# Optimization experiments

Measured on AMD Instinct MI355X. Metric: run time of the kernel, lower is better.

## Reference

```python
import jax, jax.numpy as jnp
import numpy as np

N = 20000   # nodes
G = 8       # graphs
NP = N // G # nodes per graph
DEG = 32    # avg degree = avg_num_neighbors
E = N * DEG # edges
C = 64      # channels (features_dim, hidden 0e/1o multiplicity)
S = 8       # num_species
NB = 8      # num bessel basis
L = 3       # nlayers
CUT = 6.0
AVG = 32.0


def setup_inputs() -> dict:
    rng = np.random.default_rng(0)
    # edges strictly within each graph, sender != receiver (guarantees nonzero lengths a.s.)
    il = rng.integers(0, NP, E)
    off = rng.integers(1, NP, E)
    ge = rng.integers(0, G, E)
    base = ge * NP
    edge_index = jnp.asarray(np.stack([base + il, base + (il + off) % NP]).astype(np.int64))
    batch = jnp.asarray(np.repeat(np.arange(G), NP).astype(np.int64))
    species = jnp.asarray(rng.integers(0, S, N).astype(np.int64))
    pos = jnp.asarray((rng.random((N, 3)) * 10.0).astype(np.float32))
    cell = jnp.asarray((10.0 * np.eye(3)[None] + 0.1 * rng.standard_normal((G, 3, 3))).astype(np.float32))
    Sij = jnp.asarray(rng.integers(-1, 2, (E, 3)).astype(np.float32))
    ks = jax.random.split(jax.random.key(0), 16)
    def w(k, shape, fan):
        return jax.random.normal(k, shape, jnp.float32) / np.sqrt(fan).astype(np.float32)
    return dict(
        pos=pos, cell=cell, Sij=Sij,
        W_embed=w(ks[0], (S, C), S), W_x=w(ks[1], (C, C), C),
        W_up_s=w(ks[2], (L, C, C), C), W_up_v=w(ks[3], (L, C, C), C),
        Wr1=w(ks[4], (L, NB, 64), NB), br1=jnp.zeros((L, 64), jnp.float32),
        Wr2=w(ks[5], (L, 64, 64), 64), br2=jnp.zeros((L, 64), jnp.float32),
        Wr3=w(ks[6], (L, 64, 4 * C), 64),
        W_msg_s=w(ks[7], (L, C, C), C), W_msg_v=w(ks[8], (L, C, C), C),
        W_sc_s=w(ks[9], (L, S, C, C), C), W_sc_v=w(ks[10], (L, S, C, C), C),
        W_p_s=w(ks[11], (L, C, C), C), W_p_v=w(ks[12], (L, C, C), C),
        W_read=w(ks[13], (L, 3, C), C),
        edge_index=edge_index, batch=batch, species=species,
    )


def _forward(pos, cell, Sij, W_embed, W_x, W_up_s, W_up_v, Wr1, br1, Wr2, br2, Wr3,
             W_msg_s, W_msg_v, W_sc_s, W_sc_v, W_p_s, W_p_v, W_read,
             edge_index, batch, species):
    snd, rcv = edge_index[0], edge_index[1]
    # PBC shift vectors: per-edge einsum with that edge's graph cell (== per-graph split einsum)
    shift = jnp.einsum('ei,eij->ej', Sij, cell[batch[snd]])
    Rij = (pos[rcv] - pos[snd] + shift) / CUT
    lengths = jnp.linalg.norm(Rij, axis=1)
    mask = (lengths > 0).astype(pos.dtype)  # zero-length edge masking (in place of boolean filter)
    safe = jnp.where(lengths > 0, lengths, 1.0)
    # spherical harmonics up to l=1, component normalization on unit vectors
    y1 = jnp.sqrt(3.0) * Rij / safe[:, None]
    # bessel radial basis (r_max=1 since lengths pre-scaled by cutoff) + polynomial cutoff p=2
    nfreq = jnp.arange(1, NB + 1, dtype=pos.dtype)
    bess = jnp.sqrt(2.0) * jnp.sin(jnp.pi * nfreq * safe[:, None]) / safe[:, None]
    xl = safe
    env = jnp.where(xl < 1.0, 1.0 - 6.0 * xl**2 + 8.0 * xl**3 - 3.0 * xl**4, 0.0)
    edge_feats = bess * (env * mask)[:, None]  # [E, NB]
    attrs = jax.nn.one_hot(species, S, dtype=pos.dtype)  # [N, S]
    s = attrs @ W_embed                      # scalar features [N, C]
    v = jnp.zeros((s.shape[0], C, 3), s.dtype)  # vector features [N, C, 3]
    xf = s @ W_x                             # linear_x residual features
    inv_sqrt3 = 1.0 / jnp.sqrt(3.0)
    outs = []
    for l in range(L):
        s_up = s @ W_up_s[l]
        v_up = jnp.einsum('ncm,co->nom', v, W_up_v[l])
        # radial MLP -> per-edge tensor-product path weights [E, 4, C]
        h = jax.nn.silu(edge_feats @ Wr1[l] + br1[l])
        h = jax.nn.silu(h @ Wr2[l] + br2[l])
        wts = (h @ Wr3[l]).reshape(-1, 4, C) * mask[:, None, None]
        ss, vv = s_up[snd], v_up[snd]
        # equivariant message paths: 0x0->0, 1x1->0 (dot), 0x1->1, 1x0->1
        m_s = wts[:, 0] * ss + wts[:, 1] * (jnp.einsum('ecm,em->ec', vv, y1) * inv_sqrt3)
        m_v = wts[:, 2][:, :, None] * ss[:, :, None] * y1[:, None, :] + wts[:, 3][:, :, None] * vv
        agg_s = jax.ops.segment_sum(m_s, rcv, num_segments=s.shape[0]) / AVG
        agg_v = jax.ops.segment_sum(m_v, rcv, num_segments=s.shape[0]) / AVG
        msg_s = agg_s @ W_msg_s[l]
        msg_v = jnp.einsum('ncm,co->nom', agg_v, W_msg_v[l])
        # species-conditioned skip connection (sc)
        sc_s = jnp.einsum('nk,nc,kco->no', attrs, s, W_sc_s[l])
        sc_v = jnp.einsum('nk,ncm,kco->nom', attrs, v, W_sc_v[l])
        # product block: depthwise product with x_node_feats, linear mix, + sc
        s = (xf * msg_s) @ W_p_s[l] + sc_s
        v = jnp.einsum('ncm,co->nom', xf[:, :, None] * msg_v, W_p_v[l]) + sc_v
        # readout: hidden -> 3x1o = 9 values per node
        outs.append(jnp.einsum('ncm,oc->nom', v, W_read[l]).reshape(-1, 9))
    node_e = jax.nn.silu(jnp.stack(outs, -1)).sum(-1)          # [N, 9]
    graph_e = jax.ops.segment_sum(node_e, batch, num_segments=G)
    return graph_e.reshape(G, 3, 3)


def reference(pos, cell, Sij, W_embed, W_x, W_up_s, W_up_v, Wr1, br1, Wr2, br2, Wr3,
              W_msg_s, W_msg_v, W_sc_s, W_sc_v, W_p_s, W_p_v, W_read,
              edge_index, batch, species):
    return _forward(pos, cell, Sij, W_embed, W_x, W_up_s, W_up_v, Wr1, br1, Wr2, br2, Wr3,
                    W_msg_s, W_msg_v, W_sc_s, W_sc_v, W_p_s, W_p_v, W_read,
                    edge_index, batch, species)
```

## Files before the change

### kernel.cpp

```cpp
#include <hip/hip_runtime.h>
#include <math.h>

#define NN 20000
#define GG 8
#define NPG 2500
#define EE 640000
#define EPAD 944000
#define NLAYERS 3
#define CUTR 6.0f
#define AVGN 32.0f
#define NBASIS 8
#define WPL 22528
#define RTS 88

#define LDS_HANDOFF() do { \
    asm volatile("s_waitcnt lgkmcnt(0)" ::: "memory"); \
    __builtin_amdgcn_sched_barrier(0); \
  } while (0)

typedef short bf16x8 __attribute__((ext_vector_type(8)));
typedef _Float16 f16x8 __attribute__((ext_vector_type(8)));
typedef float f32x4 __attribute__((ext_vector_type(4)));

__device__ __forceinline__ float silu_f(float x){ return x / (1.0f + __expf(-x)); }
__device__ __forceinline__ unsigned short f2h(float f){
  union { _Float16 h; unsigned short u; } x; x.h = (_Float16)f;
  return x.u;
}

__global__ void k_count(const int* __restrict__ ei, int* __restrict__ deg)
{
  int e = blockIdx.x * 256 + threadIdx.x;
  if (e >= EE) return;
  atomicAdd(&deg[ei[EE + e]], 1);
}

__global__ void k_scan(const int* __restrict__ deg, int* __restrict__ rowptrP,
                       int* __restrict__ cursor)
{
  __shared__ int buf[1024];
  __shared__ int carry;
  int tid = threadIdx.x;
  if (tid == 0) carry = 0;
  __syncthreads();
  for (int base = 0; base < NN; base += 1024) {
    int i = base + tid;
    int x = (i < NN) ? ((deg[i] + 15) & ~15) : 0;
    buf[tid] = x; __syncthreads();
    for (int off = 1; off < 1024; off <<= 1) {
      int t = (tid >= off) ? buf[tid - off] : 0;
      __syncthreads();
      buf[tid] += t;
      __syncthreads();
    }
    int incl = buf[tid];
    int c = carry;
    __syncthreads();
    if (i < NN) { rowptrP[i] = c + incl - x; cursor[i] = c + incl - x; }
    if (tid == 1023) carry = c + incl;
    __syncthreads();
  }
  if (tid == 0) rowptrP[NN] = carry;
}

__global__ void k_scatter(const int* __restrict__ ei, int* __restrict__ cursor,
                          unsigned* __restrict__ csrE)
{
  int e = blockIdx.x * 256 + threadIdx.x;
  if (e >= EE) return;
  int slot = atomicAdd(&cursor[ei[EE + e]], 1);
  csrE[slot] = (unsigned)e;
}

__global__ __launch_bounds__(512) void k_sortrows(const int* __restrict__ rowptrP,
                                                  unsigned* __restrict__ csrE)
{
  __shared__ unsigned buf[8*512];
  int w = threadIdx.x >> 6, lane = threadIdx.x & 63;
  unsigned* b = buf + w*512;
  int r = blockIdx.x*8 + w;
  int start = rowptrP[r], end = rowptrP[r+1];
  int P = end - start;
  if (P < 2 || P > 512) return;
  for (int i = lane; i < P; i += 64) b[i] = csrE[start + i];
  LDS_HANDOFF();
  for (int pass = 0; pass < P; ++pass) {
    int par = pass & 1;
    for (int i = lane; 2*i + par + 1 < P; i += 64) {
      int idx = 2*i + par;
      unsigned a = b[idx], c = b[idx+1];
      if (a > c) { b[idx] = c; b[idx+1] = a; }
    }
    LDS_HANDOFF();
  }
  for (int i = lane; i < P; i += 64) csrE[start + i] = b[i];
}

__global__ void k_geom_slot(const float* __restrict__ pos, const float* __restrict__ cell,
                            const float* __restrict__ Sij, const int* __restrict__ ei,
                            const int* __restrict__ batch, const unsigned* __restrict__ csrE,
                            unsigned short* __restrict__ efeatH, float* __restrict__ y1mP,
                            int* __restrict__ sndP)
{
  int slot = blockIdx.x * 256 + threadIdx.x;
  if (slot >= EPAD) return;
  int e = (int)csrE[slot];
  if (e < 0) {
    ((uint4*)efeatH)[slot] = make_uint4(0,0,0,0);
    ((float4*)y1mP)[slot]  = make_float4(0,0,0,0);
    sndP[slot] = 0;
    return;
  }
  int snd = ei[e], rcv = ei[EE + e];
  int g = batch[snd];
  float s0 = Sij[e*3+0], s1 = Sij[e*3+1], s2_ = Sij[e*3+2];
  const float* cg = cell + g*9;
  float R[3];
  #pragma unroll
  for (int j = 0; j < 3; ++j) {
    float shift = s0*cg[0*3+j] + s1*cg[1*3+j] + s2_*cg[2*3+j];
    R[j] = (pos[rcv*3+j] - pos[snd*3+j] + shift) * (1.0f/CUTR);
  }
  float len = sqrtf(R[0]*R[0] + R[1]*R[1] + R[2]*R[2]);
  float mk   = (len > 0.0f) ? 1.0f : 0.0f;
  float safe = (len > 0.0f) ? len  : 1.0f;
  float inv  = 1.0f / safe;
  const float sqrt3 = 1.7320508075688772f;
  float x = safe;
  float env = (x < 1.0f) ? (1.0f - 6.0f*x*x + 8.0f*x*x*x - 3.0f*x*x*x*x) : 0.0f;
  float emk = env * mk;
  const float sqrt2 = 1.4142135623730951f;
  const float PI_F = 3.14159265358979323846f;
  union { unsigned short u[8]; uint4 q; } fb;
  #pragma unroll
  for (int n = 1; n <= NBASIS; ++n)
    fb.u[n-1] = f2h(sqrt2 * __sinf(PI_F * (float)n * safe) * inv * emk);
  ((uint4*)efeatH)[slot] = fb.q;
  ((float4*)y1mP)[slot]  = make_float4(sqrt3*R[0]*inv, sqrt3*R[1]*inv, sqrt3*R[2]*inv, mk);
  sndP[slot] = snd;
}

__global__ void k_wprep(const float* __restrict__ Wr1, const float* __restrict__ Wr2,
                        const float* __restrict__ Wr3, unsigned short* __restrict__ wfrag)
{
  int gid = blockIdx.x * 256 + threadIdx.x;
  if (gid >= 3 * WPL) return;
  int l = gid / WPL, r = gid % WPL;
  float val;
  if (r < 2048) {
    int f = r >> 9, wi = r & 511, L = wi >> 3, j = wi & 7;
    int k = (L >> 4) * 8 + j, n = L & 15, ct = f;
    val = (k < 8) ? Wr1[l*512 + k*64 + ct*16 + n] : 0.0f;
  } else if (r < 6144) {
    int r2 = r - 2048;
    int f = r2 >> 9, wi = r2 & 511, L = wi >> 3, j = wi & 7;
    int kt = f >> 2, ct = f & 3;
    int k = kt*32 + (L >> 4)*8 + j, n = L & 15;
    val = Wr2[l*4096 + k*64 + ct*16 + n];
  } else {
    int r3 = r - 6144;
    int f = r3 >> 9, wi = r3 & 511, L = wi >> 3, j = wi & 7;
    int kt = f >> 4, ct = f & 15;
    int k = kt*32 + (L >> 4)*8 + j, n = L & 15;
    val = Wr3[l*16384 + k*256 + ct*16 + n];
  }
  wfrag[gid] = f2h(val);
}

__global__ void k_embed0(const int* __restrict__ species, const float* __restrict__ W_embed,
                         const float* __restrict__ W_x, const float* __restrict__ Wus0,
                         float* __restrict__ T,
                         float* __restrict__ s, float* __restrict__ v,
                         float4* __restrict__ nodeP, float* __restrict__ acc_out)
{
  if (blockIdx.x == 0) {
    for (int t = threadIdx.x; t < 512; t += 256) {
      int sp = t >> 6, o = t & 63;
      float a = 0.0f;
      for (int k = 0; k < 64; ++k) a += W_embed[sp*64 + k] * W_x[k*64 + o];
      T[t] = a;
    }
  }
  int gid = blockIdx.x * 256 + threadIdx.x;
  if (gid >= NN * 64) return;
  int n = gid >> 6, c = gid & 63;
  int sp = species[n];
  s[gid] = W_embed[sp*64 + c];
  float up = 0.0f;
  for (int k = 0; k < 64; ++k) up += W_embed[sp*64 + k] * Wus0[k*64 + c];
  nodeP[gid] = make_float4(up, 0.0f, 0.0f, 0.0f);
  #pragma unroll
  for (int m = 0; m < 3; ++m) v[(n*3 + m)*64 + c] = 0.0f;
  if (c < 9) acc_out[n*9 + c] = 0.0f;
}

__global__ __launch_bounds__(512, 2) void k_gather(
    const int* __restrict__ rowptrP,
    const unsigned short* __restrict__ efeatH, const float4* __restrict__ y1mP,
    const int* __restrict__ sndP, const float4* __restrict__ nodeP,
    const unsigned short* __restrict__ wfrag,
    const float* __restrict__ br1, const float* __restrict__ br2,
    float4* __restrict__ aggP)
{
  __shared__ unsigned short smw[WPL];
  __shared__ float smf[128];
  __shared__ unsigned short rtAll[8*16*RTS];
  __shared__ float4 ymAll[8*16];
  __shared__ int sndAll[8*16];
  int tid = threadIdx.x;
  if (tid < 64) { smf[tid] = br1[tid]; smf[64+tid] = br2[tid]; }
  {
    const unsigned* src = (const unsigned*)wfrag;
    unsigned* dst = (unsigned*)smw;
    for (int i = tid; i < WPL/2; i += 512) dst[i] = src[i];
  }
  __syncthreads();
  const unsigned short* Wr1f = smw;
  const unsigned short* Wr2f = smw + 2048;
  const unsigned short* Wr3f = smw + 6144;

  int w = tid >> 6, lane = tid & 63;
  int n16 = lane & 15, quad = lane >> 4;
  unsigned short* rt = rtAll + w*16*RTS;
  float4* ym = ymAll + w*16;
  int* sndL = sndAll + w*16;
  int g = blockIdx.x & 7, rr = (blockIdx.x >> 3)*8 + w;
  if (rr < NPG) {
  int r = g*NPG + rr;
  int start = rowptrP[r], end = rowptrP[r+1];
  float as[4] = {0,0,0,0};
  float av[4][3] = {{0,0,0},{0,0,0},{0,0,0},{0,0,0}};
  const float inv_sqrt3 = 0.5773502691896258f;

  for (int e0 = start; e0 < end; e0 += 16) {
    if (quad == 1) ym[n16] = y1mP[e0 + n16];
    if (quad == 2) sndL[n16] = sndP[e0 + n16];
    LDS_HANDOFF();
    float4 np[4][4];
    #pragma unroll
    for (int ctm = 0; ctm < 4; ++ctm)
      #pragma unroll
      for (int j = 0; j < 4; ++j)
        np[ctm][j] = nodeP[(size_t)sndL[quad*4 + j]*64 + ctm*16 + n16];
    f16x8 aef = {0,0,0,0,0,0,0,0};
    if (quad == 0)
      aef = *(const f16x8*)(efeatH + (size_t)(e0 + n16)*8);
    f32x4 hacc[4];
    #pragma unroll
    for (int ct = 0; ct < 4; ++ct) {
      f16x8 bf = *(const f16x8*)(Wr1f + (ct*64 + lane)*8);
      hacc[ct] = __builtin_amdgcn_mfma_f32_16x16x32_f16(aef, bf, (f32x4){0,0,0,0}, 0, 0, 0);
    }
    #pragma unroll
    for (int ct = 0; ct < 4; ++ct) {
      int ch = ct*16 + n16;
      float b = smf[ch];
      #pragma unroll
      for (int reg = 0; reg < 4; ++reg)
        rt[(quad*4 + reg)*RTS + ch] = f2h(silu_f(hacc[ct][reg] + b));
    }
    LDS_HANDOFF();
    f16x8 a1[2];
    #pragma unroll
    for (int kt = 0; kt < 2; ++kt)
      a1[kt] = *(const f16x8*)(rt + n16*RTS + kt*32 + quad*8);
    LDS_HANDOFF();
    #pragma unroll
    for (int ct = 0; ct < 4; ++ct) {
      f16x8 b0 = *(const f16x8*)(Wr2f + ((0*4 + ct)*64 + lane)*8);
      f16x8 b1 = *(const f16x8*)(Wr2f + ((1*4 + ct)*64 + lane)*8);
      f32x4 acc = __builtin_amdgcn_mfma_f32_16x16x32_f16(a1[0], b0, (f32x4){0,0,0,0}, 0, 0, 0);
      hacc[ct]  = __builtin_amdgcn_mfma_f32_16x16x32_f16(a1[1], b1, acc, 0, 0, 0);
    }
    #pragma unroll
    for (int ct = 0; ct < 4; ++ct) {
      int ch = ct*16 + n16;
      float b = smf[64 + ch];
      #pragma unroll
      for (int reg = 0; reg < 4; ++reg) {
        float mkr = ym[quad*4 + reg].w;
        rt[(quad*4 + reg)*RTS + ch] = f2h(silu_f(hacc[ct][reg] + b) * mkr);
      }
    }
    LDS_HANDOFF();
    f16x8 a2[2];
    #pragma unroll
    for (int kt = 0; kt < 2; ++kt)
      a2[kt] = *(const f16x8*)(rt + n16*RTS + kt*32 + quad*8);
    #pragma unroll
    for (int ctm = 0; ctm < 4; ++ctm) {
      f32x4 wacc[4];
      #pragma unroll
      for (int p = 0; p < 4; ++p) {
        int ct = p*4 + ctm;
        f32x4 acc = __builtin_amdgcn_mfma_f32_16x16x32_f16(
            a2[0], *(const f16x8*)(Wr3f + ((0*16 + ct)*64 + lane)*8), (f32x4){0,0,0,0}, 0, 0, 0);
        wacc[p] = __builtin_amdgcn_mfma_f32_16x16x32_f16(
            a2[1], *(const f16x8*)(Wr3f + ((1*16 + ct)*64 + lane)*8), acc, 0, 0, 0);
      }
      #pragma unroll
      for (int j = 0; j < 4; ++j) {
        float4 y = ym[quad*4 + j];
        float4 npv = np[ctm][j];
        float dot = npv.y*y.x + npv.z*y.y + npv.w*y.z;
        float t2 = wacc[2][j]*npv.x;
        as[ctm]    += wacc[0][j]*npv.x + wacc[1][j]*dot*inv_sqrt3;
        av[ctm][0] += t2*y.x + wacc[3][j]*npv.y;
        av[ctm][1] += t2*y.y + wacc[3][j]*npv.z;
        av[ctm][2] += t2*y.z + wacc[3][j]*npv.w;
      }
      __builtin_amdgcn_sched_barrier(0);
    }
    LDS_HANDOFF();
  }
  const float invavg = 1.0f / AVGN;
  #pragma unroll
  for (int ctm = 0; ctm < 4; ++ctm) {
    float v0 = as[ctm], v1 = av[ctm][0], v2 = av[ctm][1], v3 = av[ctm][2];
    v0 += __shfl_xor(v0, 16); v0 += __shfl_xor(v0, 32);
    v1 += __shfl_xor(v1, 16); v1 += __shfl_xor(v1, 32);
    v2 += __shfl_xor(v2, 16); v2 += __shfl_xor(v2, 32);
    v3 += __shfl_xor(v3, 16); v3 += __shfl_xor(v3, 32);
    if (quad == 0)
      aggP[(size_t)r*64 + ctm*16 + n16] =
          make_float4(v0*invavg, v1*invavg, v2*invavg, v3*invavg);
  }
  }
}

__global__ __launch_bounds__(512) void k_post(
    const float4* __restrict__ aggP, const int* __restrict__ species,
    const float* __restrict__ T,
    float* __restrict__ s, float* __restrict__ v,
    const float* __restrict__ Wms, const float* __restrict__ Wmv,
    const float* __restrict__ Wscs, const float* __restrict__ Wscv,
    const float* __restrict__ Wps, const float* __restrict__ Wpv,
    const float* __restrict__ Wread,
    const float* __restrict__ Wus_n, const float* __restrict__ Wuv_n,
    float4* __restrict__ nodeP, float* __restrict__ acc_out, int has_next)
{
  __shared__ float lds[8*1024];
  int tid = threadIdx.x; int w = tid >> 6, c = tid & 63;
  float* asb = lds + w*1024;
  float* avb = asb + 64;
  float* sob = avb + 192;
  float* vob = sob + 64;
  float* tsb = vob + 192;
  float* tvb = tsb + 64;
  float* snb = tvb + 192;
  float* vnb = snb + 64;
  int n = blockIdx.x*8 + w;
  int sp = species[n];
  float4 ag = aggP[(size_t)n*64 + c];
  asb[c] = ag.x; avb[c] = ag.y; avb[64+c] = ag.z; avb[128+c] = ag.w;
  sob[c] = s[n*64 + c];
  #pragma unroll
  for (int m = 0; m < 3; ++m) vob[m*64 + c] = v[(n*3 + m)*64 + c];
  __syncthreads();
  float ms = 0, mv0 = 0, mv1 = 0, mv2 = 0;
  for (int k = 0; k < 64; ++k) {
    float wm = Wms[k*64 + c];
    ms  += asb[k]*wm;
    float wv = Wmv[k*64 + c];
    mv0 += avb[k]*wv; mv1 += avb[64+k]*wv; mv2 += avb[128+k]*wv;
  }
  float xf = T[sp*64 + c];
  tsb[c] = xf*ms; tvb[c] = xf*mv0; tvb[64+c] = xf*mv1; tvb[128+c] = xf*mv2;
  __syncthreads();
  const float* Wss = Wscs + sp*4096;
  const float* Wsv = Wscv + sp*4096;
  float sn_ = 0, vn0 = 0, vn1 = 0, vn2 = 0;
  for (int k = 0; k < 64; ++k) {
    float wp  = Wps[k*64 + c];  sn_ += tsb[k]*wp;
    float wsc = Wss[k*64 + c];  sn_ += sob[k]*wsc;
    float wpv = Wpv[k*64 + c];
    vn0 += tvb[k]*wpv; vn1 += tvb[64+k]*wpv; vn2 += tvb[128+k]*wpv;
    float wsv = Wsv[k*64 + c];
    vn0 += vob[k]*wsv; vn1 += vob[64+k]*wsv; vn2 += vob[128+k]*wsv;
  }
  s[n*64 + c] = sn_;
  v[(n*3+0)*64 + c] = vn0; v[(n*3+1)*64 + c] = vn1; v[(n*3+2)*64 + c] = vn2;
  snb[c] = sn_; vnb[c] = vn0; vnb[64+c] = vn1; vnb[128+c] = vn2;
  __syncthreads();
  if (c < 9) {
    int o3 = c / 3, m = c % 3;
    const float* wr = Wread + o3*64;
    float a = 0.0f;
    for (int k = 0; k < 64; ++k) a += vnb[m*64 + k]*wr[k];
    acc_out[n*9 + c] += silu_f(a);
  }
  if (has_next) {
    float su = 0, u0 = 0, u1 = 0, u2 = 0;
    for (int k = 0; k < 64; ++k) {
      float wu = Wus_n[k*64 + c]; su += snb[k]*wu;
      float wv = Wuv_n[k*64 + c];
      u0 += vnb[k]*wv; u1 += vnb[64+k]*wv; u2 += vnb[128+k]*wv;
    }
    nodeP[(size_t)n*64 + c] = make_float4(su, u0, u1, u2);
  }
}

__global__ void k_final(const float* __restrict__ acc_out, float* __restrict__ out)
{
  __shared__ float red[256];
  int g = blockIdx.x / 9, j = blockIdx.x % 9;
  int tid = threadIdx.x;
  float a = 0.0f;
  for (int n = g*NPG + tid; n < (g + 1)*NPG; n += 256) a += acc_out[n*9 + j];
  red[tid] = a; __syncthreads();
  for (int off = 128; off > 0; off >>= 1) {
    if (tid < off) red[tid] += red[tid + off];
    __syncthreads();
  }
  if (tid == 0) out[g*9 + j] = red[0];
}

extern "C" void kernel_launch(void* const* d_in, const int* in_sizes, int n_in,
                              void* d_out, int out_size, void* d_ws, size_t ws_size,
                              hipStream_t stream)
{
  const float* pos     = (const float*)d_in[0];
  const float* cell    = (const float*)d_in[1];
  const float* Sij     = (const float*)d_in[2];
  const float* W_embed = (const float*)d_in[3];
  const float* W_x     = (const float*)d_in[4];
  const float* W_up_s  = (const float*)d_in[5];
  const float* W_up_v  = (const float*)d_in[6];
  const float* Wr1     = (const float*)d_in[7];
  const float* br1     = (const float*)d_in[8];
  const float* Wr2     = (const float*)d_in[9];
  const float* br2     = (const float*)d_in[10];
  const float* Wr3     = (const float*)d_in[11];
  const float* W_msg_s = (const float*)d_in[12];
  const float* W_msg_v = (const float*)d_in[13];
  const float* W_sc_s  = (const float*)d_in[14];
  const float* W_sc_v  = (const float*)d_in[15];
  const float* W_p_s   = (const float*)d_in[16];
  const float* W_p_v   = (const float*)d_in[17];
  const float* W_read  = (const float*)d_in[18];
  const int*   ei      = (const int*)d_in[19];
  const int*   batch   = (const int*)d_in[20];
  const int*   species = (const int*)d_in[21];
  float* out = (float*)d_out;

  char* ws = (char*)d_ws;
  size_t off = 0;
  auto alloc = [&](size_t bytes) -> void* {
    void* p = ws + off;
    off += (bytes + 255) & ~(size_t)255;
    return p;
  };
  unsigned short* efeatH = (unsigned short*)alloc((size_t)EPAD*8*2);
  float* y1mP    = (float*)alloc((size_t)EPAD*4*4);
  int*   sndP    = (int*)alloc((size_t)EPAD*4);
  unsigned* csrE = (unsigned*)alloc((size_t)EPAD*4);
  float* sF      = (float*)alloc((size_t)NN*64*4);
  float* vF      = (float*)alloc((size_t)NN*192*4);
  float4* nodeP  = (float4*)alloc((size_t)NN*64*16);
  float4* aggP   = (float4*)alloc((size_t)NN*64*16);
  float* acc_out = (float*)alloc((size_t)NN*9*4);
  float* T       = (float*)alloc(512*4);
  unsigned short* wfrag = (unsigned short*)alloc((size_t)3*WPL*2);
  int* deg     = (int*)alloc((size_t)NN*4);
  int* rowptrP = (int*)alloc((size_t)(NN+1)*4);
  int* cursor  = (int*)alloc((size_t)NN*4);

  hipMemsetAsync(deg, 0, (size_t)NN*4, stream);
  hipMemsetAsync(csrE, 0xFF, (size_t)EPAD*4, stream);

  k_count<<<EE/256, 256, 0, stream>>>(ei, deg);
  k_scan <<<1, 1024, 0, stream>>>(deg, rowptrP, cursor);
  k_scatter <<<EE/256, 256, 0, stream>>>(ei, cursor, csrE);
  k_sortrows<<<NN/8, 512, 0, stream>>>(rowptrP, csrE);
  k_geom_slot<<<(EPAD+255)/256, 256, 0, stream>>>(pos, cell, Sij, ei, batch, csrE,
                                                  efeatH, y1mP, sndP);
  k_wprep <<<(3*WPL)/256, 256, 0, stream>>>(Wr1, Wr2, Wr3, wfrag);
  k_embed0<<<NN*64/256, 256, 0, stream>>>(species, W_embed, W_x, W_up_s, T,
                                          sF, vF, nodeP, acc_out);

  const int GATHER_BLOCKS = 8 * ((NPG + 7) / 8);
  for (int l = 0; l < NLAYERS; ++l) {
    k_gather<<<GATHER_BLOCKS, 512, 0, stream>>>(rowptrP, efeatH, (const float4*)y1mP, sndP,
                                                nodeP, wfrag + l*WPL, br1 + l*64, br2 + l*64,
                                                aggP);
    int has_next = (l < NLAYERS-1) ? 1 : 0;
    const float* Wus_n = W_up_s + (has_next ? (l+1)*4096 : l*4096);
    const float* Wuv_n = W_up_v + (has_next ? (l+1)*4096 : l*4096);
    k_post<<<2500, 512, 0, stream>>>(aggP, species, T, sF, vF,
                                     W_msg_s + l*4096, W_msg_v + l*4096,
                                     W_sc_s + l*32768, W_sc_v + l*32768,
                                     W_p_s + l*4096, W_p_v + l*4096,
                                     W_read + l*192, Wus_n, Wuv_n,
                                     nodeP, acc_out, has_next);
  }
  k_final<<<72, 256, 0, stream>>>(acc_out, out);
}
```

Measured before the change: 1.103 ms.

## Replace per-edge radial MLP with precomputed lookup table and linear interpolation

The radial MLP (Bessel basis, two hidden layers, output weights) depends only on edge length, so it is now tabulated per layer at 4097 points in a setup kernel. The gather kernel linearly interpolates these table entries instead of running three MFMA layers per edge tile. This removes the per-edge MFMA work, the LDS weight staging and the fp16 feature buffer. In exchange it adds random table reads, a 4 MB table per layer that should stay cache-resident, and a small interpolation error.

Result: faster. 916.5 us (median of 3 runs) (-16.9%).

```diff
diff --git a/kernel.cpp b/kernel.cpp
--- a/kernel.cpp
+++ b/kernel.cpp
@@ -10,23 +10,14 @@
 #define CUTR 6.0f
 #define AVGN 32.0f
 #define NBASIS 8
-#define WPL 22528
-#define RTS 88
+#define NT 4096
 
 #define LDS_HANDOFF() do { \
     asm volatile("s_waitcnt lgkmcnt(0)" ::: "memory"); \
     __builtin_amdgcn_sched_barrier(0); \
   } while (0)
 
-typedef short bf16x8 __attribute__((ext_vector_type(8)));
-typedef _Float16 f16x8 __attribute__((ext_vector_type(8)));
-typedef float f32x4 __attribute__((ext_vector_type(4)));
-
 __device__ __forceinline__ float silu_f(float x){ return x / (1.0f + __expf(-x)); }
-__device__ __forceinline__ unsigned short f2h(float f){
-  union { _Float16 h; unsigned short u; } x; x.h = (_Float16)f;
-  return x.u;
-}
 
 __global__ void k_count(const int* __restrict__ ei, int* __restrict__ deg)
 {
@@ -99,15 +90,13 @@
 __global__ void k_geom_slot(const float* __restrict__ pos, const float* __restrict__ cell,
                             const float* __restrict__ Sij, const int* __restrict__ ei,
                             const int* __restrict__ batch, const unsigned* __restrict__ csrE,
-                            unsigned short* __restrict__ efeatH, float* __restrict__ y1mP,
-                            int* __restrict__ sndP)
+                            float* __restrict__ y1mP, int* __restrict__ sndP)
 {
   int slot = blockIdx.x * 256 + threadIdx.x;
   if (slot >= EPAD) return;
   int e = (int)csrE[slot];
   if (e < 0) {
-    ((uint4*)efeatH)[slot] = make_uint4(0,0,0,0);
-    ((float4*)y1mP)[slot]  = make_float4(0,0,0,0);
+    ((float4*)y1mP)[slot] = make_float4(0.0f, 0.0f, 0.0f, -1.0f);
     sndP[slot] = 0;
     return;
   }
@@ -122,49 +111,50 @@
     R[j] = (pos[rcv*3+j] - pos[snd*3+j] + shift) * (1.0f/CUTR);
   }
   float len = sqrtf(R[0]*R[0] + R[1]*R[1] + R[2]*R[2]);
-  float mk   = (len > 0.0f) ? 1.0f : 0.0f;
-  float safe = (len > 0.0f) ? len  : 1.0f;
+  float safe = (len > 0.0f) ? len : 1.0f;
   float inv  = 1.0f / safe;
   const float sqrt3 = 1.7320508075688772f;
-  float x = safe;
-  float env = (x < 1.0f) ? (1.0f - 6.0f*x*x + 8.0f*x*x*x - 3.0f*x*x*x*x) : 0.0f;
-  float emk = env * mk;
+  float rq = (len > 0.0f) ? fminf(len, 1.0f) : -1.0f;
+  ((float4*)y1mP)[slot] = make_float4(sqrt3*R[0]*inv, sqrt3*R[1]*inv, sqrt3*R[2]*inv, rq);
+  sndP[slot] = snd;
+}
+
+__global__ __launch_bounds__(64) void k_tab(const float* __restrict__ Wr1, const float* __restrict__ br1,
+                                            const float* __restrict__ Wr2, const float* __restrict__ br2,
+                                            const float* __restrict__ Wr3, float4* __restrict__ Twts)
+{
+  __shared__ float h1s[64], h2s[64];
+  int l  = blockIdx.x / (NT+1);
+  int ip = blockIdx.x - l*(NT+1);
+  int c  = threadIdx.x;
+  float r  = (float)ip / (float)NT;
+  float re = fmaxf(r, 1e-7f);
+  float env = (r < 1.0f) ? (1.0f - 6.0f*r*r + 8.0f*r*r*r - 3.0f*r*r*r*r) : 0.0f;
   const float sqrt2 = 1.4142135623730951f;
   const float PI_F = 3.14159265358979323846f;
-  union { unsigned short u[8]; uint4 q; } fb;
+  float ef[NBASIS];
   #pragma unroll
   for (int n = 1; n <= NBASIS; ++n)
-    fb.u[n-1] = f2h(sqrt2 * __sinf(PI_F * (float)n * safe) * inv * emk);
-  ((uint4*)efeatH)[slot] = fb.q;
-  ((float4*)y1mP)[slot]  = make_float4(sqrt3*R[0]*inv, sqrt3*R[1]*inv, sqrt3*R[2]*inv, mk);
-  sndP[slot] = snd;
-}
-
-__global__ void k_wprep(const float* __restrict__ Wr1, const float* __restrict__ Wr2,
-                        const float* __restrict__ Wr3, unsigned short* __restrict__ wfrag)
-{
-  int gid = blockIdx.x * 256 + threadIdx.x;
-  if (gid >= 3 * WPL) return;
-  int l = gid / WPL, r = gid % WPL;
-  float val;
-  if (r < 2048) {
-    int f = r >> 9, wi = r & 511, L = wi >> 3, j = wi & 7;
-    int k = (L >> 4) * 8 + j, n = L & 15, ct = f;
-    val = (k < 8) ? Wr1[l*512 + k*64 + ct*16 + n] : 0.0f;
-  } else if (r < 6144) {
-    int r2 = r - 2048;
-    int f = r2 >> 9, wi = r2 & 511, L = wi >> 3, j = wi & 7;
-    int kt = f >> 2, ct = f & 3;
-    int k = kt*32 + (L >> 4)*8 + j, n = L & 15;
-    val = Wr2[l*4096 + k*64 + ct*16 + n];
-  } else {
-    int r3 = r - 6144;
-    int f = r3 >> 9, wi = r3 & 511, L = wi >> 3, j = wi & 7;
-    int kt = f >> 4, ct = f & 15;
-    int k = kt*32 + (L >> 4)*8 + j, n = L & 15;
-    val = Wr3[l*16384 + k*256 + ct*16 + n];
-  }
-  wfrag[gid] = f2h(val);
+    ef[n-1] = sqrt2 * sinf(PI_F * (float)n * re) / re * env;
+  float a = br1[l*64 + c];
+  #pragma unroll
+  for (int k = 0; k < NBASIS; ++k) a += ef[k] * Wr1[l*512 + k*64 + c];
+  h1s[c] = a / (1.0f + expf(-a));
+  __syncthreads();
+  float b = br2[l*64 + c];
+  for (int k = 0; k < 64; ++k) b += h1s[k] * Wr2[l*4096 + k*64 + c];
+  h2s[c] = b / (1.0f + expf(-b));
+  __syncthreads();
+  float acc0 = 0, acc1 = 0, acc2 = 0, acc3 = 0;
+  for (int k = 0; k < 64; ++k) {
+    float h = h2s[k];
+    const float* wv = Wr3 + l*16384 + k*256;
+    acc0 += h * wv[0*64 + c];
+    acc1 += h * wv[1*64 + c];
+    acc2 += h * wv[2*64 + c];
+    acc3 += h * wv[3*64 + c];
+  }
+  Twts[(size_t)(l*(NT+1) + ip)*64 + c] = make_float4(acc0, acc1, acc2, acc3);
 }
 
 __global__ void k_embed0(const int* __restrict__ species, const float* __restrict__ W_embed,
@@ -196,32 +186,15 @@
 
 __global__ __launch_bounds__(512, 2) void k_gather(
     const int* __restrict__ rowptrP,
-    const unsigned short* __restrict__ efeatH, const float4* __restrict__ y1mP,
-    const int* __restrict__ sndP, const float4* __restrict__ nodeP,
-    const unsigned short* __restrict__ wfrag,
-    const float* __restrict__ br1, const float* __restrict__ br2,
+    const float4* __restrict__ y1mP, const int* __restrict__ sndP,
+    const float4* __restrict__ nodeP, const float4* __restrict__ Twts,
     float4* __restrict__ aggP)
 {
-  __shared__ unsigned short smw[WPL];
-  __shared__ float smf[128];
-  __shared__ unsigned short rtAll[8*16*RTS];
   __shared__ float4 ymAll[8*16];
   __shared__ int sndAll[8*16];
   int tid = threadIdx.x;
-  if (tid < 64) { smf[tid] = br1[tid]; smf[64+tid] = br2[tid]; }
-  {
-    const unsigned* src = (const unsigned*)wfrag;
-    unsigned* dst = (unsigned*)smw;
-    for (int i = tid; i < WPL/2; i += 512) dst[i] = src[i];
-  }
-  __syncthreads();
-  const unsigned short* Wr1f = smw;
-  const unsigned short* Wr2f = smw + 2048;
-  const unsigned short* Wr3f = smw + 6144;
-
   int w = tid >> 6, lane = tid & 63;
   int n16 = lane & 15, quad = lane >> 4;
-  unsigned short* rt = rtAll + w*16*RTS;
   float4* ym = ymAll + w*16;
   int* sndL = sndAll + w*16;
   int g = blockIdx.x & 7, rr = (blockIdx.x >> 3)*8 + w;
@@ -236,80 +209,46 @@
     if (quad == 1) ym[n16] = y1mP[e0 + n16];
     if (quad == 2) sndL[n16] = sndP[e0 + n16];
     LDS_HANDOFF();
+    float4 yj[4]; float mkj[4], fracj[4]; int idxj[4];
+    #pragma unroll
+    for (int j = 0; j < 4; ++j) {
+      float4 y = ym[quad*4 + j];
+      yj[j] = y;
+      float u = y.w;
+      mkj[j] = (u >= 0.0f) ? 1.0f : 0.0f;
+      float ppos = fmaxf(u, 0.0f) * (float)NT;
+      int idx = (int)ppos; if (idx > NT-1) idx = NT-1;
+      idxj[j] = idx;
+      fracj[j] = ppos - (float)idx;
+    }
     float4 np[4][4];
     #pragma unroll
     for (int ctm = 0; ctm < 4; ++ctm)
       #pragma unroll
       for (int j = 0; j < 4; ++j)
         np[ctm][j] = nodeP[(size_t)sndL[quad*4 + j]*64 + ctm*16 + n16];
-    f16x8 aef = {0,0,0,0,0,0,0,0};
-    if (quad == 0)
-      aef = *(const f16x8*)(efeatH + (size_t)(e0 + n16)*8);
-    f32x4 hacc[4];
-    #pragma unroll
-    for (int ct = 0; ct < 4; ++ct) {
-      f16x8 bf = *(const f16x8*)(Wr1f + (ct*64 + lane)*8);
-      hacc[ct] = __builtin_amdgcn_mfma_f32_16x16x32_f16(aef, bf, (f32x4){0,0,0,0}, 0, 0, 0);
-    }
-    #pragma unroll
-    for (int ct = 0; ct < 4; ++ct) {
-      int ch = ct*16 + n16;
-      float b = smf[ch];
-      #pragma unroll
-      for (int reg = 0; reg < 4; ++reg)
-        rt[(quad*4 + reg)*RTS + ch] = f2h(silu_f(hacc[ct][reg] + b));
-    }
-    LDS_HANDOFF();
-    f16x8 a1[2];
-    #pragma unroll
-    for (int kt = 0; kt < 2; ++kt)
-      a1[kt] = *(const f16x8*)(rt + n16*RTS + kt*32 + quad*8);
-    LDS_HANDOFF();
-    #pragma unroll
-    for (int ct = 0; ct < 4; ++ct) {
-      f16x8 b0 = *(const f16x8*)(Wr2f + ((0*4 + ct)*64 + lane)*8);
-      f16x8 b1 = *(const f16x8*)(Wr2f + ((1*4 + ct)*64 + lane)*8);
-      f32x4 acc = __builtin_amdgcn_mfma_f32_16x16x32_f16(a1[0], b0, (f32x4){0,0,0,0}, 0, 0, 0);
-      hacc[ct]  = __builtin_amdgcn_mfma_f32_16x16x32_f16(a1[1], b1, acc, 0, 0, 0);
-    }
-    #pragma unroll
-    for (int ct = 0; ct < 4; ++ct) {
-      int ch = ct*16 + n16;
-      float b = smf[64 + ch];
-      #pragma unroll
-      for (int reg = 0; reg < 4; ++reg) {
-        float mkr = ym[quad*4 + reg].w;
-        rt[(quad*4 + reg)*RTS + ch] = f2h(silu_f(hacc[ct][reg] + b) * mkr);
-      }
-    }
-    LDS_HANDOFF();
-    f16x8 a2[2];
-    #pragma unroll
-    for (int kt = 0; kt < 2; ++kt)
-      a2[kt] = *(const f16x8*)(rt + n16*RTS + kt*32 + quad*8);
     #pragma unroll
     for (int ctm = 0; ctm < 4; ++ctm) {
-      f32x4 wacc[4];
-      #pragma unroll
-      for (int p = 0; p < 4; ++p) {
-        int ct = p*4 + ctm;
-        f32x4 acc = __builtin_amdgcn_mfma_f32_16x16x32_f16(
-            a2[0], *(const f16x8*)(Wr3f + ((0*16 + ct)*64 + lane)*8), (f32x4){0,0,0,0}, 0, 0, 0);
-        wacc[p] = __builtin_amdgcn_mfma_f32_16x16x32_f16(
-            a2[1], *(const f16x8*)(Wr3f + ((1*16 + ct)*64 + lane)*8), acc, 0, 0, 0);
-      }
       #pragma unroll
       for (int j = 0; j < 4; ++j) {
-        float4 y = ym[quad*4 + j];
+        const float4* tp = Twts + (size_t)idxj[j]*64 + ctm*16 + n16;
+        float4 t0 = tp[0];
+        float4 t1 = tp[64];
+        float f = fracj[j], mk = mkj[j];
+        float4 wp;
+        wp.x = mk*(t0.x + f*(t1.x - t0.x));
+        wp.y = mk*(t0.y + f*(t1.y - t0.y));
+        wp.z = mk*(t0.z + f*(t1.z - t0.z));
+        wp.w = mk*(t0.w + f*(t1.w - t0.w));
+        float4 y = yj[j];
         float4 npv = np[ctm][j];
         float dot = npv.y*y.x + npv.z*y.y + npv.w*y.z;
-        float t2 = wacc[2][j]*npv.x;
-        as[ctm]    += wacc[0][j]*npv.x + wacc[1][j]*dot*inv_sqrt3;
-        av[ctm][0] += t2*y.x + wacc[3][j]*npv.y;
-        av[ctm][1] += t2*y.y + wacc[3][j]*npv.z;
-        av[ctm][2] += t2*y.z + wacc[3][j]*npv.w;
+        float t2 = wp.z*npv.x;
+        as[ctm]    += wp.x*npv.x + wp.y*dot*inv_sqrt3;
+        av[ctm][0] += t2*y.x + wp.w*npv.y;
+        av[ctm][1] += t2*y.y + wp.w*npv.z;
+        av[ctm][2] += t2*y.z + wp.w*npv.w;
       }
-      __builtin_amdgcn_sched_barrier(0);
     }
     LDS_HANDOFF();
   }
@@ -450,7 +389,6 @@
     off += (bytes + 255) & ~(size_t)255;
     return p;
   };
-  unsigned short* efeatH = (unsigned short*)alloc((size_t)EPAD*8*2);
   float* y1mP    = (float*)alloc((size_t)EPAD*4*4);
   int*   sndP    = (int*)alloc((size_t)EPAD*4);
   unsigned* csrE = (unsigned*)alloc((size_t)EPAD*4);
@@ -460,7 +398,7 @@
   float4* aggP   = (float4*)alloc((size_t)NN*64*16);
   float* acc_out = (float*)alloc((size_t)NN*9*4);
   float* T       = (float*)alloc(512*4);
-  unsigned short* wfrag = (unsigned short*)alloc((size_t)3*WPL*2);
+  float4* Twts   = (float4*)alloc((size_t)NLAYERS*(NT+1)*64*16);
   int* deg     = (int*)alloc((size_t)NN*4);
   int* rowptrP = (int*)alloc((size_t)(NN+1)*4);
   int* cursor  = (int*)alloc((size_t)NN*4);
@@ -473,16 +411,15 @@
   k_scatter <<<EE/256, 256, 0, stream>>>(ei, cursor, csrE);
   k_sortrows<<<NN/8, 512, 0, stream>>>(rowptrP, csrE);
   k_geom_slot<<<(EPAD+255)/256, 256, 0, stream>>>(pos, cell, Sij, ei, batch, csrE,
-                                                  efeatH, y1mP, sndP);
-  k_wprep <<<(3*WPL)/256, 256, 0, stream>>>(Wr1, Wr2, Wr3, wfrag);
+                                                  y1mP, sndP);
+  k_tab<<<NLAYERS*(NT+1), 64, 0, stream>>>(Wr1, br1, Wr2, br2, Wr3, Twts);
   k_embed0<<<NN*64/256, 256, 0, stream>>>(species, W_embed, W_x, W_up_s, T,
                                           sF, vF, nodeP, acc_out);
 
   const int GATHER_BLOCKS = 8 * ((NPG + 7) / 8);
   for (int l = 0; l < NLAYERS; ++l) {
-    k_gather<<<GATHER_BLOCKS, 512, 0, stream>>>(rowptrP, efeatH, (const float4*)y1mP, sndP,
-                                                nodeP, wfrag + l*WPL, br1 + l*64, br2 + l*64,
-                                                aggP);
+    k_gather<<<GATHER_BLOCKS, 512, 0, stream>>>(rowptrP, (const float4*)y1mP, sndP,
+                                                nodeP, Twts + (size_t)l*(NT+1)*64, aggP);
     int has_next = (l < NLAYERS-1) ? 1 : 0;
     const float* Wus_n = W_up_s + (has_next ? (l+1)*4096 : l*4096);
     const float* Wuv_n = W_up_v + (has_next ? (l+1)*4096 : l*4096);
```
